# Kernel optimization log

Hardware: AMD Instinct MI355X
Metric: run time of the kernel (lower is better)

## Reference

```python
import jax, jax.numpy as jnp
import numpy as np
from jax import lax

B, F_BINS, T = 4, 196, 1000
DM, H, DEPTH, FFN, L, EDIM = 512, 8, 64, 2048, 4, 128


def setup_inputs() -> dict:
    key = jax.random.key(0)
    ks = jax.random.split(key, 16)
    d = {}
    d['spec'] = jax.random.normal(ks[0], (B, 1, F_BINS, T), jnp.float32)
    d['conv1_w'] = jax.random.normal(ks[1], (32, 1, 5, 5), jnp.float32) / 5.0
    d['conv1_b'] = jax.random.normal(ks[2], (32,), jnp.float32) * 0.01
    d['conv2_w'] = jax.random.normal(ks[3], (64, 32, 5, 5), jnp.float32) / np.sqrt(32 * 25)
    d['conv2_b'] = jax.random.normal(ks[4], (64,), jnp.float32) * 0.01
    d['proj_w'] = jax.random.normal(ks[5], (DM, 64), jnp.float32) / 8.0
    d['proj_b'] = jnp.zeros((DM,), jnp.float32)
    d['ln1_g'] = jnp.ones((L, DM), jnp.float32)
    d['ln1_b'] = jnp.zeros((L, DM), jnp.float32)
    s = 1.0 / np.sqrt(DM)
    for i, nm in enumerate(['qw', 'kw', 'vw', 'dw']):
        d[nm] = jax.random.normal(ks[6 + i], (L, DM, DM), jnp.float32) * s
    for nm in ['qb', 'kb', 'vb', 'db']:
        d[nm] = jnp.zeros((L, DM), jnp.float32)
    d['Er'] = jax.random.normal(ks[10], (L, T, DEPTH), jnp.float32)
    d['ln2_g'] = jnp.ones((L, DM), jnp.float32)
    d['ln2_b'] = jnp.zeros((L, DM), jnp.float32)
    d['f1w'] = jax.random.normal(ks[11], (L, FFN, DM), jnp.float32) * s
    d['f1b'] = jnp.zeros((L, FFN), jnp.float32)
    d['f2w'] = jax.random.normal(ks[12], (L, DM, FFN), jnp.float32) / np.sqrt(FFN)
    d['f2b'] = jnp.zeros((L, DM), jnp.float32)
    d['deproj_w'] = jax.random.normal(ks[13], (EDIM, DM), jnp.float32) * s
    d['deproj_b'] = jnp.zeros((EDIM,), jnp.float32)
    return d


def _layernorm(x, g, b, eps=1e-5):
    mu = jnp.mean(x, -1, keepdims=True)
    var = jnp.mean(jnp.square(x - mu), -1, keepdims=True)
    return g * (x - mu) / jnp.sqrt(var + eps) + b


def _skew(QEr):
    # QEr: [B,H,S,S] -> music-transformer skew trick
    b, h, s, _ = QEr.shape
    padded = jnp.pad(QEr, ((0, 0), (0, 0), (0, 0), (1, 0)))  # [B,H,S,S+1]
    return padded.reshape(b, h, s + 1, s)[:, :, 1:, :]


def _forward(spec, conv1_w, conv1_b, conv2_w, conv2_b, proj_w, proj_b,
             ln1_g, ln1_b, qw, qb, kw, kb, vw, vb, dw, db, Er,
             ln2_g, ln2_b, f1w, f1b, f2w, f2b, deproj_w, deproj_b):
    dn = ('NCHW', 'OIHW', 'NCHW')
    x = lax.conv_general_dilated(spec, conv1_w, (1, 1), 'SAME', dimension_numbers=dn)
    x = jax.nn.gelu(x + conv1_b[None, :, None, None], approximate=False)
    x = lax.reduce_window(x, -jnp.inf, lax.max, (1, 1, 14, 1), (1, 1, 14, 1), 'VALID')
    x = lax.conv_general_dilated(x, conv2_w, (1, 1), 'SAME', dimension_numbers=dn)
    x = jax.nn.gelu(x + conv2_b[None, :, None, None], approximate=False)
    x = lax.reduce_window(x, -jnp.inf, lax.max, (1, 1, 14, 1), (1, 1, 14, 1), 'VALID')
    x = x.reshape(B, 64, T)              # freq collapsed to 1, flatten(1,2)
    x = x.transpose(0, 2, 1)             # [B,T,64]
    x = x @ proj_w.T + proj_b            # [B,T,DM]
    scale = 1.0 / np.sqrt(DEPTH)
    for l in range(L):
        xn = _layernorm(x, ln1_g[l], ln1_b[l])
        Q = (xn @ qw[l].T + qb[l]).reshape(B, T, H, DEPTH).transpose(0, 2, 1, 3)
        K = (xn @ kw[l].T + kb[l]).reshape(B, T, H, DEPTH).transpose(0, 2, 1, 3)
        V = (xn @ vw[l].T + vb[l]).reshape(B, T, H, DEPTH).transpose(0, 2, 1, 3)
        QEr = jnp.einsum('bhsd,rd->bhsr', Q, Er[l])        # relative pos scores
        Srel = _skew(QEr)
        logits = (jnp.einsum('bhsd,bhtd->bhst', Q, K) + Srel) * scale
        attn = jax.nn.softmax(logits, axis=-1)
        out = jnp.einsum('bhst,bhtd->bhsd', attn, V)
        out = out.transpose(0, 2, 1, 3).reshape(B, T, DM)
        x = x + (out @ dw[l].T + db[l])
        xn2 = _layernorm(x, ln2_g[l], ln2_b[l])
        ff = jax.nn.relu(xn2 @ f1w[l].T + f1b[l]) @ f2w[l].T + f2b[l]
        x = x + ff
    return x @ deproj_w.T + deproj_b     # [B,T,EDIM]


def reference(spec, conv1_w, conv1_b, conv2_w, conv2_b, proj_w, proj_b,
              ln1_g, ln1_b, qw, qb, kw, kb, vw, vb, dw, db, Er,
              ln2_g, ln2_b, f1w, f1b, f2w, f2b, deproj_w, deproj_b):
    return _forward(spec, conv1_w, conv1_b, conv2_w, conv2_b, proj_w, proj_b,
                    ln1_g, ln1_b, qw, qb, kw, kb, vw, vb, dw, db, Er,
                    ln2_g, ln2_b, f1w, f1b, f2w, f2b, deproj_w, deproj_b)
```

## Files before the change

### kernel.cpp

```cpp
#include <hip/hip_runtime.h>
#include <hip/hip_bf16.h>
#include <hip/hip_fp16.h>
#include <math.h>

#define BB 4
#define FBINS 196
#define TT 1000
#define DM 512
#define HH 8
#define DEPTH 64
#define FFN 2048
#define LL 4
#define EDIM 128
#define BT (BB*TT)
#define PSHIFT 12.0f

typedef __hip_bfloat16 bf16;
typedef __attribute__((ext_vector_type(8))) short short8;
typedef __attribute__((ext_vector_type(4))) float floatx4;

#define ARENA_BYTES 420000000ULL
static void* g_arena = nullptr;
__attribute__((constructor)) static void arena_init() {
    if (!g_arena) (void)hipMalloc(&g_arena, ARENA_BYTES);
}

__device__ __forceinline__ float gelu_f(float x) {
    return 0.5f * x * (1.0f + erff(x * 0.70710678118654752440f));
}

__global__ __launch_bounds__(256) void sniff_k(const unsigned short* __restrict__ p,
                                               int n, int* __restrict__ cnt) {
    int i = blockIdx.x * 256 + threadIdx.x;
    int c = 0;
    for (; i < n; i += gridDim.x * 256) {
        unsigned short u = p[i];
        if ((unsigned short)(u & 0x7FFF) > (unsigned short)0x7F80) c++;
    }
    if (c) atomicAdd(cnt, c);
}

#define NCVT 17
struct CvtArgs {
    const void* src[NCVT];
    unsigned dst[NCVT];
    unsigned cum[NCVT + 1];
    const int* cnt;
    float* dstA;
};
__global__ __launch_bounds__(256) void cvt_all(CvtArgs a) {
    unsigned i = blockIdx.x * 256 + threadIdx.x;
    if (i >= a.cum[NCVT]) return;
    bool isb = (*a.cnt == 0);
    int w = 0;
    while (i >= a.cum[w + 1]) w++;
    unsigned j = i - a.cum[w];
    float v = isb ? __bfloat162float(((const bf16*)a.src[w])[j])
                  : ((const float*)a.src[w])[j];
    a.dstA[a.dst[w] + j] = v;
}

__global__ __launch_bounds__(256) void f2bf_dyn(const void* __restrict__ src,
                                                bf16* __restrict__ d, int n,
                                                const int* __restrict__ cnt) {
    int i = blockIdx.x * 256 + threadIdx.x;
    if (i >= n) return;
    if (*cnt == 0) d[i] = ((const bf16*)src)[i];
    else           d[i] = __float2bfloat16(((const float*)src)[i]);
}

__global__ __launch_bounds__(256) void w2perm(const void* __restrict__ src,
                                              bf16* __restrict__ d,
                                              const int* __restrict__ cnt) {
    int idx = blockIdx.x * 256 + threadIdx.x;
    if (idx >= 51200) return;
    int c = idx / 800, k = idx - c * 800;
    int kc = k >> 5, ci = k & 31;
    int di = kc / 5, dj = kc - di * 5;
    int s = ((c * 32 + ci) * 5 + di) * 5 + dj;
    float v = (*cnt == 0) ? __bfloat162float(((const bf16*)src)[s])
                          : ((const float*)src)[s];
    d[idx] = __float2bfloat16(v);
}

__global__ __launch_bounds__(256) void conv1_pool2(const float* __restrict__ spec,
                                                   const float* __restrict__ w1,
                                                   const float* __restrict__ b1,
                                                   bf16* __restrict__ P1c) {
    __shared__ float ss[18][256];
    __shared__ float sw[200];
    int jt = blockIdx.x, p = blockIdx.y, z = blockIdx.z;
    int b = z >> 2, cg = z & 3;
    int tid = threadIdx.x;
    for (int i = tid; i < 200; i += 256) sw[i] = w1[cg * 200 + i];
    int ibase = p * 14, c0 = jt * 250 - 2;
    for (int idx = tid; idx < 18 * 256; idx += 256) {
        int rr = idx >> 8, cc = idx & 255;
        int gi = ibase - 2 + rr, gj = c0 + cc;
        ss[rr][cc] = (gi >= 0 && gi < FBINS && gj >= 0 && gj < TT && cc < 254)
                         ? spec[(size_t)b * FBINS * TT + (size_t)gi * TT + gj] : 0.f;
    }
    __syncthreads();
    if (tid >= 250) return;
    int j = jt * 250 + tid;
    unsigned short* orow = (unsigned short*)P1c + ((size_t)((b * 14 + p) * 1000 + j)) * 32;
    for (int cpl = 0; cpl < 8; cpl += 2) {
        int cp = cg * 8 + cpl;
        float conv[2][14];
        float b0 = b1[cp], b1v = b1[cp + 1];
#pragma unroll
        for (int i = 0; i < 14; i++) { conv[0][i] = b0; conv[1][i] = b1v; }
        const float* w0 = sw + cpl * 25;
        const float* w1p = sw + (cpl + 1) * 25;
        for (int rr = 0; rr < 18; rr++) {
            float v0 = ss[rr][tid], v1 = ss[rr][tid + 1], v2 = ss[rr][tid + 2],
                  v3 = ss[rr][tid + 3], v4 = ss[rr][tid + 4];
#pragma unroll
            for (int di = 0; di < 5; di++) {
                int i = rr - di;
                if (i >= 0 && i < 14) {
                    conv[0][i] += v0 * w0[di * 5] + v1 * w0[di * 5 + 1] + v2 * w0[di * 5 + 2]
                                + v3 * w0[di * 5 + 3] + v4 * w0[di * 5 + 4];
                    conv[1][i] += v0 * w1p[di * 5] + v1 * w1p[di * 5 + 1] + v2 * w1p[di * 5 + 2]
                                + v3 * w1p[di * 5 + 3] + v4 * w1p[di * 5 + 4];
                }
            }
        }
        float m0 = -1e30f, m1 = -1e30f;
#pragma unroll
        for (int i = 0; i < 14; i++) {
            m0 = fmaxf(m0, gelu_f(conv[0][i]));
            m1 = fmaxf(m1, gelu_f(conv[1][i]));
        }
        bf16 mb0 = __float2bfloat16(m0), mb1 = __float2bfloat16(m1);
        unsigned pk = ((unsigned)(*(unsigned short*)&mb1) << 16) |
                      (unsigned)(*(unsigned short*)&mb0);
        *(unsigned*)(orow + cp) = pk;
    }
}

__global__ __launch_bounds__(256) void conv2_gemm(const bf16* __restrict__ P1c,
                                                  const bf16* __restrict__ W2p,
                                                  const float* __restrict__ c2b,
                                                  bf16* __restrict__ convout) {
    __shared__ __align__(16) short Asm[64 * 40];
    __shared__ __align__(16) short Bsm[64 * 40];
    int tid = threadIdx.x, wave = tid >> 6, lane = tid & 63;
    int q = lane >> 4, l15 = lane & 15;
    int jt = blockIdx.x, i = blockIdx.y, b = blockIdx.z;
    int lrow = tid >> 2, lci = (tid & 3) * 8;
    int jrow = jt * 64 + lrow;
    int mw = (wave & 1) * 32, nw = (wave >> 1) * 32;
    floatx4 acc[2][2] = {};
    for (int di = 0; di < 5; di++) {
        int ii = i + di - 2;
        bool iok = (ii >= 0 && ii < 14);
        for (int dj = 0; dj < 5; dj++) {
            int kc = di * 5 + dj;
            {
                int jj = jrow + dj - 2;
                uint4 v = make_uint4(0u, 0u, 0u, 0u);
                if (iok && jrow < TT && jj >= 0 && jj < TT)
                    v = *(const uint4*)(P1c +
                        (((size_t)(b * 14 + ii)) * TT + jj) * 32 + lci);
                *(uint4*)(Asm + lrow * 40 + lci) = v;
            }
            {
                *(uint4*)(Bsm + lrow * 40 + lci) =
                    *(const uint4*)(W2p + (size_t)lrow * 800 + kc * 32 + lci);
            }
            __syncthreads();
            short8 a0 = *(const short8*)(Asm + (mw + l15) * 40 + q * 8);
            short8 a1 = *(const short8*)(Asm + (mw + 16 + l15) * 40 + q * 8);
            short8 b0 = *(const short8*)(Bsm + (nw + l15) * 40 + q * 8);
            short8 b1 = *(const short8*)(Bsm + (nw + 16 + l15) * 40 + q * 8);
            acc[0][0] = __builtin_amdgcn_mfma_f32_16x16x32_bf16(a0, b0, acc[0][0], 0, 0, 0);
            acc[0][1] = __builtin_amdgcn_mfma_f32_16x16x32_bf16(a0, b1, acc[0][1], 0, 0, 0);
            acc[1][0] = __builtin_amdgcn_mfma_f32_16x16x32_bf16(a1, b0, acc[1][0], 0, 0, 0);
            acc[1][1] = __builtin_amdgcn_mfma_f32_16x16x32_bf16(a1, b1, acc[1][1], 0, 0, 0);
            __syncthreads();
        }
    }
#pragma unroll
    for (int im = 0; im < 2; im++) {
#pragma unroll
        for (int jn = 0; jn < 2; jn++) {
            int c = nw + jn * 16 + l15;
            float bv = c2b[c];
#pragma unroll
            for (int r = 0; r < 4; r++) {
                int j = jt * 64 + mw + im * 16 + q * 4 + r;
                if (j >= TT) continue;
                convout[((size_t)(b * 14 + i) * TT + j) * 64 + c] =
                    __float2bfloat16(acc[im][jn][r] + bv);
            }
        }
    }
}

__global__ __launch_bounds__(256) void pool2_k(const bf16* __restrict__ convout,
                                               bf16* __restrict__ p2t) {
    int idx = blockIdx.x * 256 + threadIdx.x;
    if (idx >= 256000) return;
    int c = idx & 63, bj = idx >> 6;
    int b = bj / 1000, j = bj - b * 1000;
    float m = -1e30f;
#pragma unroll
    for (int i = 0; i < 14; i++)
        m = fmaxf(m, gelu_f(__bfloat162float(convout[((size_t)(b * 14 + i) * 1000 + j) * 64 + c])));
    p2t[(size_t)bj * 64 + c] = __float2bfloat16(m);
}

__global__ __launch_bounds__(256) void layernorm_k(const float* __restrict__ x,
                                                   const float* __restrict__ g,
                                                   const float* __restrict__ bta,
                                                   bf16* __restrict__ y) {
    __shared__ float red[256];
    int row = blockIdx.x, tid = threadIdx.x;
    const float* xr = x + (size_t)row * DM;
    float v0 = xr[tid], v1 = xr[tid + 256];
    red[tid] = v0 + v1;
    __syncthreads();
    for (int s = 128; s > 0; s >>= 1) { if (tid < s) red[tid] += red[tid + s]; __syncthreads(); }
    float mu = red[0] * (1.f / 512.f);
    __syncthreads();
    float d0 = v0 - mu, d1 = v1 - mu;
    red[tid] = d0 * d0 + d1 * d1;
    __syncthreads();
    for (int s = 128; s > 0; s >>= 1) { if (tid < s) red[tid] += red[tid + s]; __syncthreads(); }
    float rstd = rsqrtf(red[0] * (1.f / 512.f) + 1e-5f);
    bf16* yr = y + (size_t)row * DM;
    yr[tid]       = __float2bfloat16(d0 * rstd * g[tid]       + bta[tid]);
    yr[tid + 256] = __float2bfloat16(d1 * rstd * g[tid + 256] + bta[tid + 256]);
}

__global__ __launch_bounds__(256) void gemm_out(const float* __restrict__ A,
                                                const float* __restrict__ B,
                                                const float* __restrict__ bias,
                                                const int* __restrict__ cnt,
                                                void* __restrict__ dout,
                                                int M, int N, int K) {
    __shared__ float As[32][33];
    __shared__ float Bs[32][33];
    int tid = threadIdx.x;
    int tx = tid & 15, ty = tid >> 4;
    int m0 = blockIdx.x * 32, n0 = blockIdx.y * 32;
    float c[2][2] = {};
    for (int k0 = 0; k0 < K; k0 += 32) {
#pragma unroll
        for (int i = 0; i < 4; i++) {
            int idx = i * 256 + tid;
            int r = idx >> 5, kk = idx & 31;
            int gm = m0 + r;
            As[r][kk] = (gm < M) ? A[(size_t)gm * K + k0 + kk] : 0.f;
            Bs[r][kk] = B[(size_t)(n0 + r) * K + k0 + kk];
        }
        __syncthreads();
#pragma unroll
        for (int k = 0; k < 32; k++) {
            float a0 = As[ty * 2][k], a1 = As[ty * 2 + 1][k];
            float b0 = Bs[tx * 2][k], b1 = Bs[tx * 2 + 1][k];
            c[0][0] += a0 * b0; c[0][1] += a0 * b1;
            c[1][0] += a1 * b0; c[1][1] += a1 * b1;
        }
        __syncthreads();
    }
    bool isb = (*cnt == 0);
#pragma unroll
    for (int i = 0; i < 2; i++) {
        int m = m0 + ty * 2 + i;
        if (m >= M) continue;
#pragma unroll
        for (int jj = 0; jj < 2; jj++) {
            int n = n0 + tx * 2 + jj;
            float v = c[i][jj] + bias[n];
            if (isb) ((bf16*)dout)[(size_t)m * N + n] = __float2bfloat16(v);
            else     ((float*)dout)[(size_t)m * N + n] = v;
        }
    }
}

template <int BM, int NT, int ROUTE, int ACT, bool OUT_BF16>
__global__ __launch_bounds__(256) void mfma_big(const bf16* __restrict__ A,
                                                const bf16* __restrict__ B,
                                                const float* __restrict__ bias,
                                                const float* __restrict__ resid,
                                                float* __restrict__ Cf,
                                                bf16* __restrict__ Cb,
                                                int M, int N, int K,
                                                size_t wstride, int bstride,
                                                size_t ostride) {
    __shared__ __align__(16) short Asm[BM * 40];
    __shared__ __align__(16) short Bsm[NT * 40];
    int tid = threadIdx.x, wave = tid >> 6, lane = tid & 63;
    int q = lane >> 4, l15 = lane & 15;
    int m0 = blockIdx.x * BM, n0 = blockIdx.y * NT;
    int lrow = tid >> 2, lk = (tid & 3) * 8;
    constexpr int MF = (NT == 128) ? (BM / 16) : (BM / 32);
    int m0w = (NT == 128) ? 0 : ((wave >> 1) * (BM / 2));
    int nfb = (NT == 128) ? (wave * 32) : ((wave & 1) * 32);
    floatx4 acc[MF][2] = {};
    for (int k0 = 0; k0 < K; k0 += 32) {
#pragma unroll
        for (int hh = 0; hh < BM / 64; hh++) {
            int row = lrow + hh * 64, gm = m0 + row;
            uint4 v = make_uint4(0u, 0u, 0u, 0u);
            if (gm < M) v = *(const uint4*)(A + (size_t)gm * K + k0 + lk);
            *(uint4*)(Asm + row * 40 + lk) = v;
        }
#pragma unroll
        for (int hh = 0; hh < NT / 64; hh++) {
            int row = lrow + hh * 64, gn = n0 + row;
            const bf16* src = ROUTE
                ? B + (size_t)(gn >> 9) * wstride + (size_t)(gn & 511) * K + k0 + lk
                : B + (size_t)gn * K + k0 + lk;
            *(uint4*)(Bsm + row * 40 + lk) = *(const uint4*)src;
        }
        __syncthreads();
        short8 a[MF], b2[2];
#pragma unroll
        for (int im = 0; im < MF; im++)
            a[im] = *(const short8*)(Asm + (m0w + im * 16 + l15) * 40 + q * 8);
#pragma unroll
        for (int jn = 0; jn < 2; jn++)
            b2[jn] = *(const short8*)(Bsm + (nfb + jn * 16 + l15) * 40 + q * 8);
#pragma unroll
        for (int im = 0; im < MF; im++)
#pragma unroll
            for (int jn = 0; jn < 2; jn++)
                acc[im][jn] = __builtin_amdgcn_mfma_f32_16x16x32_bf16(
                    a[im], b2[jn], acc[im][jn], 0, 0, 0);
        __syncthreads();
    }
#pragma unroll
    for (int im = 0; im < MF; im++) {
#pragma unroll
        for (int jn = 0; jn < 2; jn++) {
            int nn = n0 + nfb + jn * 16 + l15;
            float bval = ROUTE ? bias[(nn >> 9) * bstride + (nn & 511)] : bias[nn];
#pragma unroll
            for (int r = 0; r < 4; r++) {
                int m = m0 + m0w + im * 16 + q * 4 + r;
                if (m >= M) continue;
                float v = acc[im][jn][r] + bval;
                if (resid) v += resid[(size_t)m * N + nn];
                if (ACT == 1) v = fmaxf(v, 0.f);
                if (ROUTE)
                    Cb[(size_t)(nn >> 9) * ostride + (size_t)m * 512 + (nn & 511)] =
                        __float2bfloat16(v);
                else if (OUT_BF16)
                    Cb[(size_t)m * N + nn] = __float2bfloat16(v);
                else
                    Cf[(size_t)m * N + nn] = v;
            }
        }
    }
}

__global__ __launch_bounds__(256) void vt_k(const bf16* __restrict__ Vb,
                                            bf16* __restrict__ Vt) {
    __shared__ short tile[64][65];
    int t0 = blockIdx.x * 64, z = blockIdx.y;
    int b = z >> 3, h = z & 7;
    int tid = threadIdx.x;
#pragma unroll
    for (int i = 0; i < 16; i++) {
        int tr = i * 4 + (tid >> 6), d = tid & 63;
        int t = t0 + tr;
        bf16 v = (t < TT) ? Vb[((size_t)b * TT + t) * DM + h * 64 + d] : (bf16)__float2bfloat16(0.f);
        tile[tr][d] = *(short*)&v;
    }
    __syncthreads();
#pragma unroll
    for (int i = 0; i < 16; i++) {
        int dr = i * 4 + (tid >> 6), tc = tid & 63;
        *(short*)&Vt[(size_t)z * 65536 + dr * 1024 + t0 + tc] = tile[tc][dr];
    }
}

__global__ __launch_bounds__(256) void qer_mfma(const bf16* __restrict__ Q,
                                                const bf16* __restrict__ Er,
                                                bf16* __restrict__ QErB) {
    __shared__ __align__(16) short Asm[64 * 40];
    __shared__ __align__(16) short Bsm[128 * 40];
    int tid = threadIdx.x;
    int wave = tid >> 6, lane = tid & 63;
    int q = lane >> 4, l15 = lane & 15;
    int m0 = blockIdx.x * 64, n0 = blockIdx.y * 128;
    int z = blockIdx.z, b = z >> 3, h = z & 7;
    const bf16* Ap = Q + (size_t)b * TT * DM + h * 64;
    int lrow = tid >> 2, lk = (tid & 3) * 8;
    floatx4 acc[4][2] = {};
    for (int k0 = 0; k0 < 64; k0 += 32) {
        {
            int gm = m0 + lrow;
            uint4 v = make_uint4(0u, 0u, 0u, 0u);
            if (gm < TT) v = *(const uint4*)(Ap + (size_t)gm * DM + k0 + lk);
            *(uint4*)(Asm + lrow * 40 + lk) = v;
        }
        {
            int gn = n0 + lrow;
            uint4 v0 = make_uint4(0u, 0u, 0u, 0u), v1 = v0;
            if (gn < TT)      v0 = *(const uint4*)(Er + (size_t)gn * 64 + k0 + lk);
            if (gn + 64 < TT) v1 = *(const uint4*)(Er + (size_t)(gn + 64) * 64 + k0 + lk);
            *(uint4*)(Bsm + lrow * 40 + lk) = v0;
            *(uint4*)(Bsm + (lrow + 64) * 40 + lk) = v1;
        }
        __syncthreads();
        short8 a[4], bf[2];
#pragma unroll
        for (int im = 0; im < 4; im++)
            a[im] = *(const short8*)(Asm + (im * 16 + l15) * 40 + q * 8);
#pragma unroll
        for (int jn = 0; jn < 2; jn++)
            bf[jn] = *(const short8*)(Bsm + (wave * 32 + jn * 16 + l15) * 40 + q * 8);
#pragma unroll
        for (int im = 0; im < 4; im++)
#pragma unroll
            for (int jn = 0; jn < 2; jn++)
                acc[im][jn] = __builtin_amdgcn_mfma_f32_16x16x32_bf16(
                    a[im], bf[jn], acc[im][jn], 0, 0, 0);
        __syncthreads();
    }
    bf16* Cz = QErB + (size_t)z * 1000000;
#pragma unroll
    for (int im = 0; im < 4; im++) {
#pragma unroll
        for (int jn = 0; jn < 2; jn++) {
            int n = n0 + wave * 32 + jn * 16 + l15;
            if (n >= TT) continue;
#pragma unroll
            for (int r = 0; r < 4; r++) {
                int m = m0 + im * 16 + q * 4 + r;
                if (m < TT) Cz[(size_t)m * TT + n] = __float2bfloat16(acc[im][jn][r]);
            }
        }
    }
}

__global__ __launch_bounds__(256) void score_mfma(const bf16* __restrict__ Q,
                                                  const bf16* __restrict__ K,
                                                  const bf16* __restrict__ QErB,
                                                  __half* __restrict__ Sc) {
    __shared__ __align__(16) short Asm[64 * 40];
    __shared__ __align__(16) short Bsm[128 * 40];
    int tid = threadIdx.x;
    int wave = tid >> 6, lane = tid & 63;
    int q = lane >> 4, l15 = lane & 15;
    int m0 = blockIdx.x * 64, n0 = blockIdx.y * 128;
    int z = blockIdx.z, b = z >> 3, h = z & 7;
    const bf16* Ap = Q + (size_t)b * TT * DM + h * 64;
    const bf16* Bp = K + (size_t)b * TT * DM + h * 64;
    int lrow = tid >> 2, lk = (tid & 3) * 8;
    floatx4 acc[4][2] = {};
    for (int k0 = 0; k0 < 64; k0 += 32) {
        {
            int gm = m0 + lrow;
            uint4 v = make_uint4(0u, 0u, 0u, 0u);
            if (gm < TT) v = *(const uint4*)(Ap + (size_t)gm * DM + k0 + lk);
            *(uint4*)(Asm + lrow * 40 + lk) = v;
        }
        {
            int gn = n0 + lrow;
            uint4 v0 = make_uint4(0u, 0u, 0u, 0u), v1 = v0;
            if (gn < TT)      v0 = *(const uint4*)(Bp + (size_t)gn * DM + k0 + lk);
            if (gn + 64 < TT) v1 = *(const uint4*)(Bp + (size_t)(gn + 64) * DM + k0 + lk);
            *(uint4*)(Bsm + lrow * 40 + lk) = v0;
            *(uint4*)(Bsm + (lrow + 64) * 40 + lk) = v1;
        }
        __syncthreads();
        short8 a[4], bf[2];
#pragma unroll
        for (int im = 0; im < 4; im++)
            a[im] = *(const short8*)(Asm + (im * 16 + l15) * 40 + q * 8);
#pragma unroll
        for (int jn = 0; jn < 2; jn++)
            bf[jn] = *(const short8*)(Bsm + (wave * 32 + jn * 16 + l15) * 40 + q * 8);
#pragma unroll
        for (int im = 0; im < 4; im++)
#pragma unroll
            for (int jn = 0; jn < 2; jn++)
                acc[im][jn] = __builtin_amdgcn_mfma_f32_16x16x32_bf16(
                    a[im], bf[jn], acc[im][jn], 0, 0, 0);
        __syncthreads();
    }
    const bf16* Ez = QErB + (size_t)z * 1000000;
    __half* Cz = Sc + (size_t)z * 1024000;
#pragma unroll
    for (int im = 0; im < 4; im++) {
#pragma unroll
        for (int jn = 0; jn < 2; jn++) {
            int n = n0 + wave * 32 + jn * 16 + l15;
            if (n >= TT) continue;
#pragma unroll
            for (int r = 0; r < 4; r++) {
                int m = m0 + im * 16 + q * 4 + r;
                if (m >= TT) continue;
                float rel;
                if (n == m + 1)  rel = 0.f;
                else if (n <= m) rel = __bfloat162float(Ez[(size_t)m * TT + (TT - 1 - m + n)]);
                else             rel = __bfloat162float(Ez[(size_t)(m + 1) * TT + (n - m - 2)]);
                Cz[(size_t)m * 1024 + n] = __float2half((acc[im][jn][r] + rel) * 0.125f);
            }
        }
    }
}

__global__ __launch_bounds__(512) void pv_mfma(const __half* __restrict__ Sc,
                                               const bf16* __restrict__ Vt,
                                               bf16* __restrict__ AO) {
    __shared__ __align__(16) short Asm[64 * 72];
    __shared__ __align__(16) short Vs[64 * 72];
    __shared__ float rowsum[64];
    __shared__ float Oc[4][16][64];
    int tid = threadIdx.x, wave = tid >> 6, lane = tid & 63;
    int q = lane >> 4, l15 = lane & 15;
    int mw = (wave & 3) * 16, kh = wave >> 2;
    int m0 = blockIdx.x * 64;
    int z = blockIdx.z, b = z >> 3, h = z & 7;
    const __half* Ap = Sc + (size_t)z * 1024000;
    const bf16* Bp = Vt + (size_t)z * 65536;
    int lrow = tid >> 3, c = (tid & 7) * 8;
    int chf = c >> 5, cc = c & 31;
    int gm = m0 + lrow;
    bool rowok = (gm < TT);
    float psum = 0.f;
    floatx4 acc[4] = {};
    for (int kb = 0; kb < 512; kb += 32) {
        int t = kb + chf * 512 + cc;
        {
            __attribute__((aligned(16))) short pv8[8];
            if (rowok && t < TT) {
                uint4 u = *(const uint4*)(Ap + (size_t)gm * 1024 + t);
                const __half2* h2 = (const __half2*)&u;
#pragma unroll
                for (int e = 0; e < 4; e++) {
                    float lo = __expf(__low2float(h2[e]) - PSHIFT);
                    float hi = __expf(__high2float(h2[e]) - PSHIFT);
                    psum += lo + hi;
                    bf16 p0 = __float2bfloat16(lo), p1 = __float2bfloat16(hi);
                    pv8[2 * e] = *(short*)&p0; pv8[2 * e + 1] = *(short*)&p1;
                }
            } else {
#pragma unroll
                for (int e = 0; e < 8; e++) pv8[e] = 0;
            }
            *(uint4*)(Asm + lrow * 72 + c) = *(uint4*)pv8;
        }
        *(uint4*)(Vs + lrow * 72 + c) = *(const uint4*)(Bp + (size_t)lrow * 1024 + t);
        __syncthreads();
        short8 a = *(const short8*)(Asm + (mw + l15) * 72 + kh * 32 + q * 8);
#pragma unroll
        for (int jn = 0; jn < 4; jn++) {
            short8 bv = *(const short8*)(Vs + (jn * 16 + l15) * 72 + kh * 32 + q * 8);
            acc[jn] = __builtin_amdgcn_mfma_f32_16x16x32_bf16(a, bv, acc[jn], 0, 0, 0);
        }
        __syncthreads();
    }
    psum += __shfl_xor(psum, 1, 64);
    psum += __shfl_xor(psum, 2, 64);
    psum += __shfl_xor(psum, 4, 64);
    if ((tid & 7) == 0) rowsum[lrow] = psum;
    if (kh == 1) {
#pragma unroll
        for (int jn = 0; jn < 4; jn++)
#pragma unroll
            for (int r = 0; r < 4; r++)
                Oc[wave & 3][q * 4 + r][jn * 16 + l15] = acc[jn][r];
    }
    __syncthreads();
    if (kh == 0) {
#pragma unroll
        for (int r = 0; r < 4; r++) {
            int lm = mw + q * 4 + r;
            int m = m0 + lm;
            if (m >= TT) continue;
            float inv = 1.f / rowsum[lm];
#pragma unroll
            for (int jn = 0; jn < 4; jn++) {
                float o = acc[jn][r] + Oc[wave & 3][q * 4 + r][jn * 16 + l15];
                AO[((size_t)b * TT + m) * DM + h * 64 + jn * 16 + l15] =
                    __float2bfloat16(o * inv);
            }
        }
    }
}

extern "C" void kernel_launch(void* const* d_in, const int* in_sizes, int n_in,
                              void* d_out, int out_size, void* d_ws, size_t ws_size,
                              hipStream_t stream) {
    if (!g_arena) (void)hipMalloc(&g_arena, ARENA_BYTES);
    float* A = (float*)g_arena;

    static const unsigned off[27] = {
        0, 784000, 784800, 784832, 836032, 836096, 868864, 869376, 871424,
        873472, 1922048, 2970624, 4019200, 5067776, 5069824, 5071872,
        5073920, 5075968, 5331968, 5334016, 5336064, 9530368, 9538560,
        13732864, 13734912, 13800448, 13800576};
    const float* spec  = A + off[0];
    const float* c1w   = A + off[1];
    const float* c1b   = A + off[2];
    const float* c2b   = A + off[4];
    const float* projb = A + off[6];
    const float* ln1g  = A + off[7];
    const float* ln1b  = A + off[8];
    const float* qb    = A + off[13];
    const float* db    = A + off[16];
    const float* ln2g  = A + off[18];
    const float* ln2b  = A + off[19];
    const float* f1b   = A + off[21];
    const float* f2b_  = A + off[23];
    const float* depw  = A + off[24];
    const float* depb  = A + off[25];

    const size_t PA = 13800576;
    float* x    = A + PA;
    float* P1   = x + 2048000;
    float* SM   = P1 + 1792000;
    bf16* P1c     = (bf16*)P1;
    bf16* p2t_b   = (bf16*)SM;
    bf16* projw_b = (bf16*)(SM + 128000);
    bf16* w2p     = (bf16*)(SM + 150000);
    int*   cnt  = (int*)(SM + 256000);
    float* ScF  = SM + 256004;
    __half* Sch = (__half*)ScF;
    float* B0   = ScF + 32000000;
    bf16* wb_qkvd = (bf16*)B0;
    bf16* wb_f1   = (bf16*)(B0 + 2097152);
    bf16* wb_f2   = (bf16*)(B0 + 4194304);
    bf16* Erb     = (bf16*)(B0 + 6291456);
    bf16* xn_b    = (bf16*)(B0 + 6419456);
    bf16* AO_b    = (bf16*)(B0 + 7443456);
    bf16* Qb_b    = (bf16*)(B0 + 8467456);
    bf16* Kb_b    = (bf16*)(B0 + 9491456);
    bf16* Vb_b    = (bf16*)(B0 + 10515456);
    bf16* FFH_b   = (bf16*)(B0 + 11539456);
    bf16* Vt      = (bf16*)(B0 + 15635456);
    bf16* QErB_b  = (bf16*)(B0 + 16684032);
    bf16* convout = QErB_b;

    hipMemsetAsync(cnt, 0, sizeof(int), stream);
    sniff_k<<<1024, 256, 0, stream>>>((const unsigned short*)d_in[20], 1000000, cnt);

    static const int cvt_ids[NCVT] = {0, 1, 2, 4, 6, 7, 8, 13, 14, 15, 16,
                                      18, 19, 21, 23, 24, 25};
    CvtArgs ca;
    unsigned cum = 0;
    for (int t = 0; t < NCVT; t++) {
        int w = cvt_ids[t];
        ca.src[t] = d_in[w];
        ca.dst[t] = off[w];
        ca.cum[t] = cum;
        cum += off[w + 1] - off[w];
    }
    ca.cum[NCVT] = cum;
    ca.cnt = cnt; ca.dstA = A;
    cvt_all<<<(cum + 255) / 256, 256, 0, stream>>>(ca);

    for (int t = 0; t < 4; t++)
        f2bf_dyn<<<4096, 256, 0, stream>>>(d_in[9 + t], wb_qkvd + (size_t)t * 1048576,
                                           1048576, cnt);
    f2bf_dyn<<<16384, 256, 0, stream>>>(d_in[20], wb_f1, 4194304, cnt);
    f2bf_dyn<<<16384, 256, 0, stream>>>(d_in[22], wb_f2, 4194304, cnt);
    f2bf_dyn<<<1000,  256, 0, stream>>>(d_in[17], Erb,   256000, cnt);
    f2bf_dyn<<<128,   256, 0, stream>>>(d_in[5],  projw_b, 32768, cnt);
    w2perm<<<200, 256, 0, stream>>>(d_in[3], w2p, cnt);

    conv1_pool2<<<dim3(4, 14, 16), 256, 0, stream>>>(spec, c1w, c1b, P1c);
    conv2_gemm<<<dim3(16, 14, 4), 256, 0, stream>>>(P1c, w2p, c2b, convout);
    pool2_k<<<1000, 256, 0, stream>>>(convout, p2t_b);
    mfma_big<64, 64, 0, 0, false><<<dim3(63, 8), 256, 0, stream>>>(
        p2t_b, projw_b, projb, nullptr, x, nullptr, BT, DM, 64, 0, 0, 0);

    for (int l = 0; l < LL; l++) {
        layernorm_k<<<BT, 256, 0, stream>>>(x, ln1g + l * DM, ln1b + l * DM, xn_b);
        mfma_big<128, 128, 1, 0, true><<<dim3(32, 12), 256, 0, stream>>>(
            xn_b, wb_qkvd + (size_t)l * DM * DM, qb + l * DM, nullptr,
            nullptr, Qb_b, BT, 1536, DM, 1048576, 2048, 2048000);
        vt_k<<<dim3(16, 32), 256, 0, stream>>>(Vb_b, Vt);
        qer_mfma<<<dim3(16, 8, 32), 256, 0, stream>>>(Qb_b, Erb + (size_t)l * TT * DEPTH, QErB_b);
        score_mfma<<<dim3(16, 8, 32), 256, 0, stream>>>(Qb_b, Kb_b, QErB_b, Sch);
        pv_mfma<<<dim3(16, 1, 32), 512, 0, stream>>>(Sch, Vt, AO_b);
        mfma_big<64, 64, 0, 0, false><<<dim3(63, 8), 256, 0, stream>>>(
            AO_b, wb_qkvd + 3 * 1048576 + (size_t)l * DM * DM, db + l * DM, x,
            x, nullptr, BT, DM, DM, 0, 0, 0);
        layernorm_k<<<BT, 256, 0, stream>>>(x, ln2g + l * DM, ln2b + l * DM, xn_b);
        mfma_big<128, 128, 0, 1, true><<<dim3(32, 16), 256, 0, stream>>>(
            xn_b, wb_f1 + (size_t)l * FFN * DM, f1b + l * FFN, nullptr,
            nullptr, FFH_b, BT, FFN, DM, 0, 0, 0);
        mfma_big<64, 64, 0, 0, false><<<dim3(63, 8), 256, 0, stream>>>(
            FFH_b, wb_f2 + (size_t)l * DM * FFN, f2b_ + l * DM, x,
            x, nullptr, BT, DM, FFN, 0, 0, 0);
    }

    gemm_out<<<dim3(125, 4), 256, 0, stream>>>(x, depw, depb, cnt, d_out, BT, EDIM, DM);
}
```

Measured before the change: 1.260 ms.

## Fuse relative-position QEr computation into score kernel with diagonal Er tile

```diff
diff --git a/kernel.cpp b/kernel.cpp
--- a/kernel.cpp
+++ b/kernel.cpp
@@ -378,72 +378,15 @@
     }
 }
 
-__global__ __launch_bounds__(256) void qer_mfma(const bf16* __restrict__ Q,
-                                                const bf16* __restrict__ Er,
-                                                bf16* __restrict__ QErB) {
-    __shared__ __align__(16) short Asm[64 * 40];
-    __shared__ __align__(16) short Bsm[128 * 40];
-    int tid = threadIdx.x;
-    int wave = tid >> 6, lane = tid & 63;
-    int q = lane >> 4, l15 = lane & 15;
-    int m0 = blockIdx.x * 64, n0 = blockIdx.y * 128;
-    int z = blockIdx.z, b = z >> 3, h = z & 7;
-    const bf16* Ap = Q + (size_t)b * TT * DM + h * 64;
-    int lrow = tid >> 2, lk = (tid & 3) * 8;
-    floatx4 acc[4][2] = {};
-    for (int k0 = 0; k0 < 64; k0 += 32) {
-        {
-            int gm = m0 + lrow;
-            uint4 v = make_uint4(0u, 0u, 0u, 0u);
-            if (gm < TT) v = *(const uint4*)(Ap + (size_t)gm * DM + k0 + lk);
-            *(uint4*)(Asm + lrow * 40 + lk) = v;
-        }
-        {
-            int gn = n0 + lrow;
-            uint4 v0 = make_uint4(0u, 0u, 0u, 0u), v1 = v0;
-            if (gn < TT)      v0 = *(const uint4*)(Er + (size_t)gn * 64 + k0 + lk);
-            if (gn + 64 < TT) v1 = *(const uint4*)(Er + (size_t)(gn + 64) * 64 + k0 + lk);
-            *(uint4*)(Bsm + lrow * 40 + lk) = v0;
-            *(uint4*)(Bsm + (lrow + 64) * 40 + lk) = v1;
-        }
-        __syncthreads();
-        short8 a[4], bf[2];
-#pragma unroll
-        for (int im = 0; im < 4; im++)
-            a[im] = *(const short8*)(Asm + (im * 16 + l15) * 40 + q * 8);
-#pragma unroll
-        for (int jn = 0; jn < 2; jn++)
-            bf[jn] = *(const short8*)(Bsm + (wave * 32 + jn * 16 + l15) * 40 + q * 8);
-#pragma unroll
-        for (int im = 0; im < 4; im++)
-#pragma unroll
-            for (int jn = 0; jn < 2; jn++)
-                acc[im][jn] = __builtin_amdgcn_mfma_f32_16x16x32_bf16(
-                    a[im], bf[jn], acc[im][jn], 0, 0, 0);
-        __syncthreads();
-    }
-    bf16* Cz = QErB + (size_t)z * 1000000;
-#pragma unroll
-    for (int im = 0; im < 4; im++) {
-#pragma unroll
-        for (int jn = 0; jn < 2; jn++) {
-            int n = n0 + wave * 32 + jn * 16 + l15;
-            if (n >= TT) continue;
-#pragma unroll
-            for (int r = 0; r < 4; r++) {
-                int m = m0 + im * 16 + q * 4 + r;
-                if (m < TT) Cz[(size_t)m * TT + n] = __float2bfloat16(acc[im][jn][r]);
-            }
-        }
-    }
-}
-
 __global__ __launch_bounds__(256) void score_mfma(const bf16* __restrict__ Q,
                                                   const bf16* __restrict__ K,
-                                                  const bf16* __restrict__ QErB,
+                                                  const bf16* __restrict__ Er,
                                                   __half* __restrict__ Sc) {
-    __shared__ __align__(16) short Asm[64 * 40];
-    __shared__ __align__(16) short Bsm[128 * 40];
+    __shared__ __align__(16) short SH[16000];
+    short* Asm = SH;
+    short* Bsm = SH + 3200;
+    short* Esm = SH + 8320;
+    short* Gl  = SH;
     int tid = threadIdx.x;
     int wave = tid >> 6, lane = tid & 63;
     int q = lane >> 4, l15 = lane & 15;
@@ -452,13 +395,22 @@
     const bf16* Ap = Q + (size_t)b * TT * DM + h * 64;
     const bf16* Bp = K + (size_t)b * TT * DM + h * 64;
     int lrow = tid >> 2, lk = (tid & 3) * 8;
-    floatx4 acc[4][2] = {};
+    int db = n0 - m0 - 64;
+    floatx4 accS[4][2] = {};
+    floatx4 accG[5][3] = {};
     for (int k0 = 0; k0 < 64; k0 += 32) {
         {
             int gm = m0 + lrow;
             uint4 v = make_uint4(0u, 0u, 0u, 0u);
             if (gm < TT) v = *(const uint4*)(Ap + (size_t)gm * DM + k0 + lk);
             *(uint4*)(Asm + lrow * 40 + lk) = v;
+            if (tid < 64) {
+                int rr = 64 + (tid >> 2);
+                int g2 = m0 + rr;
+                uint4 v2 = make_uint4(0u, 0u, 0u, 0u);
+                if (g2 < TT) v2 = *(const uint4*)(Ap + (size_t)g2 * DM + k0 + lk);
+                *(uint4*)(Asm + rr * 40 + lk) = v2;
+            }
         }
         {
             int gn = n0 + lrow;
@@ -468,23 +420,58 @@
             *(uint4*)(Bsm + lrow * 40 + lk) = v0;
             *(uint4*)(Bsm + (lrow + 64) * 40 + lk) = v1;
         }
-        __syncthreads();
-        short8 a[4], bf[2];
+        {
+#pragma unroll
+            for (int hh = 0; hh < 3; hh++) {
+                int dd = lrow + hh * 64;
+                int dl = db + dd;
+                int src = (dl <= 0) ? (999 + dl) : (dl - 1);
+                uint4 v = make_uint4(0u, 0u, 0u, 0u);
+                if (src >= 0 && src < TT)
+                    v = *(const uint4*)(Er + (size_t)src * 64 + k0 + lk);
+                *(uint4*)(Esm + dd * 40 + lk) = v;
+            }
+        }
+        __syncthreads();
+        short8 a[5], bk[2], e[3];
+#pragma unroll
+        for (int im = 0; im < 5; im++)
+            a[im] = *(const short8*)(Asm + (im * 16 + l15) * 40 + q * 8);
+#pragma unroll
+        for (int jn = 0; jn < 2; jn++)
+            bk[jn] = *(const short8*)(Bsm + (wave * 32 + jn * 16 + l15) * 40 + q * 8);
+#pragma unroll
+        for (int jg = 0; jg < 3; jg++)
+            e[jg] = *(const short8*)(Esm + (wave * 48 + jg * 16 + l15) * 40 + q * 8);
 #pragma unroll
         for (int im = 0; im < 4; im++)
-            a[im] = *(const short8*)(Asm + (im * 16 + l15) * 40 + q * 8);
-#pragma unroll
-        for (int jn = 0; jn < 2; jn++)
-            bf[jn] = *(const short8*)(Bsm + (wave * 32 + jn * 16 + l15) * 40 + q * 8);
-#pragma unroll
-        for (int im = 0; im < 4; im++)
 #pragma unroll
             for (int jn = 0; jn < 2; jn++)
-                acc[im][jn] = __builtin_amdgcn_mfma_f32_16x16x32_bf16(
-                    a[im], bf[jn], acc[im][jn], 0, 0, 0);
-        __syncthreads();
-    }
-    const bf16* Ez = QErB + (size_t)z * 1000000;
+                accS[im][jn] = __builtin_amdgcn_mfma_f32_16x16x32_bf16(
+                    a[im], bk[jn], accS[im][jn], 0, 0, 0);
+#pragma unroll
+        for (int im = 0; im < 5; im++)
+#pragma unroll
+            for (int jg = 0; jg < 3; jg++)
+                accG[im][jg] = __builtin_amdgcn_mfma_f32_16x16x32_bf16(
+                    a[im], e[jg], accG[im][jg], 0, 0, 0);
+        __syncthreads();
+    }
+#pragma unroll
+    for (int im = 0; im < 5; im++)
+#pragma unroll
+        for (int jg = 0; jg < 3; jg++) {
+            int col = wave * 48 + jg * 16 + l15;
+#pragma unroll
+            for (int r = 0; r < 4; r++) {
+                int row = im * 16 + q * 4 + r;
+                if (row < 65) {
+                    bf16 gv = __float2bfloat16(accG[im][jg][r]);
+                    Gl[row * 200 + col] = *(short*)&gv;
+                }
+            }
+        }
+    __syncthreads();
     __half* Cz = Sc + (size_t)z * 1024000;
 #pragma unroll
     for (int im = 0; im < 4; im++) {
@@ -496,11 +483,14 @@
             for (int r = 0; r < 4; r++) {
                 int m = m0 + im * 16 + q * 4 + r;
                 if (m >= TT) continue;
-                float rel;
-                if (n == m + 1)  rel = 0.f;
-                else if (n <= m) rel = __bfloat162float(Ez[(size_t)m * TT + (TT - 1 - m + n)]);
-                else             rel = __bfloat162float(Ez[(size_t)(m + 1) * TT + (n - m - 2)]);
-                Cz[(size_t)m * 1024 + n] = __float2half((acc[im][jn][r] + rel) * 0.125f);
+                float rel = 0.f;
+                if (n != m + 1) {
+                    int u = (n <= m) ? m : (m + 1);
+                    int dd = n - u - db;
+                    short gs = Gl[(u - m0) * 200 + dd];
+                    rel = __bfloat162float(*(bf16*)&gs);
+                }
+                Cz[(size_t)m * 1024 + n] = __float2half((accS[im][jn][r] + rel) * 0.125f);
             }
         }
     }
@@ -636,8 +626,7 @@
     bf16* Vb_b    = (bf16*)(B0 + 10515456);
     bf16* FFH_b   = (bf16*)(B0 + 11539456);
     bf16* Vt      = (bf16*)(B0 + 15635456);
-    bf16* QErB_b  = (bf16*)(B0 + 16684032);
-    bf16* convout = QErB_b;
+    bf16* convout = (bf16*)(B0 + 16684032);
 
     hipMemsetAsync(cnt, 0, sizeof(int), stream);
     sniff_k<<<1024, 256, 0, stream>>>((const unsigned short*)d_in[20], 1000000, cnt);
@@ -678,8 +667,8 @@
             xn_b, wb_qkvd + (size_t)l * DM * DM, qb + l * DM, nullptr,
             nullptr, Qb_b, BT, 1536, DM, 1048576, 2048, 2048000);
         vt_k<<<dim3(16, 32), 256, 0, stream>>>(Vb_b, Vt);
-        qer_mfma<<<dim3(16, 8, 32), 256, 0, stream>>>(Qb_b, Erb + (size_t)l * TT * DEPTH, QErB_b);
-        score_mfma<<<dim3(16, 8, 32), 256, 0, stream>>>(Qb_b, Kb_b, QErB_b, Sch);
+        score_mfma<<<dim3(16, 8, 32), 256, 0, stream>>>(
+            Qb_b, Kb_b, Erb + (size_t)l * TT * DEPTH, Sch);
         pv_mfma<<<dim3(16, 1, 32), 512, 0, stream>>>(Sch, Vt, AO_b);
         mfma_big<64, 64, 0, 0, false><<<dim3(63, 8), 256, 0, stream>>>(
             AO_b, wb_qkvd + 3 * 1048576 + (size_t)l * DM * DM, db + l * DM, x,
```

After: 1.169 ms. 7.2% less time.
